# Kernel optimization log

Hardware: AMD Instinct MI355X
Metric: run time of the kernel (lower is better)

The kernel has to match this reference:

```python
import jax, jax.numpy as jnp
import numpy as np

N_CELLS = 50000
DEG = 32
NNZ = N_CELLS * DEG
D_IN = 64
D_OUT = 64
NEG_SLOPE = 0.2


def setup_inputs() -> dict:
    key = jax.random.key(0)
    k0, k1, k2, k3, k4 = jax.random.split(key, 5)
    x_source = jax.random.normal(k0, (N_CELLS, D_IN), jnp.float32)
    # COO indices of the sparse neighborhood matrix N: DEG entries per row
    edge_rows = jnp.repeat(jnp.arange(N_CELLS, dtype=jnp.int32), DEG)
    edge_cols = jax.random.randint(k1, (NNZ,), 0, N_CELLS, dtype=jnp.int32)
    neighborhood_values = jax.random.uniform(k2, (NNZ,), jnp.float32)
    # xavier_uniform-ish scales (exact init irrelevant for correctness baseline)
    W0 = jax.random.normal(k3, (D_IN, D_OUT), jnp.float32) * (1.414 / np.sqrt(D_IN))
    a0 = jax.random.normal(k4, (2 * D_OUT, 1), jnp.float32) * 0.1
    return {
        "x_source": x_source,
        "edge_rows": edge_rows,
        "edge_cols": edge_cols,
        "neighborhood_values": neighborhood_values,
        "W0": W0,
        "a0": a0,
    }


def reference(x_source, edge_rows, edge_cols, neighborhood_values, W0, a0):
    # message = X W_p  : [n_cells, d_out]
    message = x_source @ W0
    d = message.shape[1]
    # [X_i || X_j] a  ==  (X_i a_src) + (X_j a_dst); compute node-level dot first,
    # then gather per edge (avoids materializing [nnz, 2d] concat)
    a_src = a0[:d, 0]
    a_dst = a0[d:, 0]
    node_src = message @ a_src  # [n_cells]
    node_dst = message @ a_dst  # [n_cells]
    e = jax.nn.leaky_relu(node_src[edge_rows] + node_dst[edge_cols],
                          negative_slope=NEG_SLOPE)  # [nnz]
    # sparse_row_norm: divide each edge value by its row sum (softmax=False path)
    row_sum = jax.ops.segment_sum(e, edge_rows, num_segments=N_CELLS)
    att = e / row_sum[edge_rows]
    # Hadamard product N^1 \odot A_1, then SpMM with message
    vals = neighborhood_values * att  # [nnz]
    out = jax.ops.segment_sum(vals[:, None] * message[edge_cols], edge_rows,
                              num_segments=N_CELLS)  # [n_cells, d_out]
    # update_func='relu'
    return jax.nn.relu(out)
```

## Files before the change

kernel.cpp:

```cpp
#include <hip/hip_runtime.h>
#include <hip/hip_fp16.h>

#define N_CELLS 50000
#define DEG 32
#define DIM 64
#define NEG_SLOPE 0.2
#define NPAIRS (N_CELLS / 2)

__global__ __launch_bounds__(256)
void gat_prep(const float* __restrict__ x,
              const float* __restrict__ W0,
              const float* __restrict__ a0,
              __half* __restrict__ x2,
              double* __restrict__ ns,
              double* __restrict__ nd) {
  __shared__ double2 p_s[DIM];

  const int tid = threadIdx.x;
  if (tid < DIM) {
    double ps = 0.0, pd = 0.0;
    const float4* w4 = (const float4*)(W0 + tid * DIM);
#pragma unroll
    for (int q = 0; q < DIM / 4; ++q) {
      float4 w = w4[q];
      ps = fma((double)w.x, (double)a0[4 * q + 0], ps);
      ps = fma((double)w.y, (double)a0[4 * q + 1], ps);
      ps = fma((double)w.z, (double)a0[4 * q + 2], ps);
      ps = fma((double)w.w, (double)a0[4 * q + 3], ps);
      pd = fma((double)w.x, (double)a0[DIM + 4 * q + 0], pd);
      pd = fma((double)w.y, (double)a0[DIM + 4 * q + 1], pd);
      pd = fma((double)w.z, (double)a0[DIM + 4 * q + 2], pd);
      pd = fma((double)w.w, (double)a0[DIM + 4 * q + 3], pd);
    }
    p_s[tid] = make_double2(ps, pd);
  }
  __syncthreads();

  const int r = blockIdx.x * 256 + tid;
  if (r >= N_CELLS) return;

  const float4* x4 = (const float4*)(x + (size_t)r * DIM);
  double s0 = 0.0, s1 = 0.0, d0 = 0.0, d1 = 0.0;
  __half2 hbuf[DIM / 2];
#pragma unroll
  for (int q = 0; q < DIM / 4; ++q) {
    float4 v = x4[q];
    double2 p0 = p_s[4 * q + 0], p1 = p_s[4 * q + 1];
    double2 p2 = p_s[4 * q + 2], p3 = p_s[4 * q + 3];
    s0 = fma((double)v.x, p0.x, s0); d0 = fma((double)v.x, p0.y, d0);
    s1 = fma((double)v.y, p1.x, s1); d1 = fma((double)v.y, p1.y, d1);
    s0 = fma((double)v.z, p2.x, s0); d0 = fma((double)v.z, p2.y, d0);
    s1 = fma((double)v.w, p3.x, s1); d1 = fma((double)v.w, p3.y, d1);
    hbuf[2 * q + 0] = __float22half2_rn(make_float2(v.x, v.y));
    hbuf[2 * q + 1] = __float22half2_rn(make_float2(v.z, v.w));
  }
  ns[r] = s0 + s1;
  nd[r] = d0 + d1;

  const uint4* src = (const uint4*)hbuf;
  uint4* p2v = (uint4*)(x2 + (size_t)r * DIM);
#pragma unroll
  for (int i = 0; i < 8; ++i) p2v[i] = src[i];
}

__global__ __launch_bounds__(256, 4)
void gat_edges(const __half* __restrict__ x2,
               const int* __restrict__ ecol,
               const float* __restrict__ nv,
               const float* __restrict__ W0,
               const double* __restrict__ ns,
               const double* __restrict__ nd,
               float* __restrict__ out) {
  __shared__ __align__(16) float w_s[4][2][DEG];
  __shared__ __align__(16) int c_s[4][2][DEG];
  __shared__ __align__(16) float h_s[4][2][2][DIM];

  const int lane = threadIdx.x & 63;
  const int wid = threadIdx.x >> 6;
  const int half = lane >> 5;
  const int sub = lane & 31;

  float w0c[DIM];
#pragma unroll
  for (int k = 0; k < DIM; ++k) w0c[k] = W0[k * DIM + lane];

  const int gwave = blockIdx.x * 4 + wid;
  const int nwaves = gridDim.x * 4;
  const unsigned* xp = (const unsigned*)x2;

  int col_c = 0; float nv_c = 0.0f; double nd_c = 0.0, ns_c = 0.0;
  if (gwave < NPAIRS) {
    const int eidx = 2 * gwave * DEG + lane;
    col_c = __builtin_nontemporal_load(ecol + eidx);
    nv_c = __builtin_nontemporal_load(nv + eidx);
    nd_c = nd[col_c];
    ns_c = ns[2 * gwave + half];
  }

  int buf = 0;
  for (int p = gwave; p < NPAIRS; p += nwaves, buf ^= 1) {
    const int r0 = 2 * p;
    const int col = col_c;
    const float nvv = nv_c;
    const double ndv = nd_c;
    const double nsv = ns_c;

    double z = nsv + ndv;
    double e = (z >= 0.0) ? z : NEG_SLOPE * z;
    double rs = e;
#pragma unroll
    for (int m = 16; m >= 1; m >>= 1) rs += __shfl_xor(rs, m, 64);
    w_s[wid][half][sub] = nvv * ((float)e / (float)rs);
    c_s[wid][half][sub] = col;

    const int pn = p + nwaves;
    const int psafe = (pn < NPAIRS) ? pn : p;
    const int eidxn = 2 * psafe * DEG + lane;
    col_c = __builtin_nontemporal_load(ecol + eidxn);
    nv_c = __builtin_nontemporal_load(nv + eidxn);
    ns_c = ns[2 * psafe + half];

    const int* cs = c_s[wid][half];
    const float* wsp = w_s[wid][half];
    float ax = 0.0f, ay = 0.0f;
#pragma unroll
    for (int b = 0; b < DEG; b += 16) {
      unsigned pk[16];
#pragma unroll
      for (int i = 0; i < 16; ++i)
        pk[i] = xp[(size_t)cs[b + i] * (DIM / 2) + sub];
#pragma unroll
      for (int i = 0; i < 16; ++i) {
        float2 v = __half22float2(*(const __half2*)&pk[i]);
        float w = wsp[b + i];
        ax = fmaf(w, v.x, ax);
        ay = fmaf(w, v.y, ay);
      }
    }
    ((float2*)h_s[wid][buf][half])[sub] = make_float2(ax, ay);

    nd_c = nd[col_c];

    float oA = 0.0f, oB = 0.0f;
    const float4* hA = (const float4*)h_s[wid][buf][0];
    const float4* hB = (const float4*)h_s[wid][buf][1];
#pragma unroll
    for (int q = 0; q < DIM / 4; ++q) {
      float4 a = hA[q];
      float4 b = hB[q];
      oA = fmaf(a.x, w0c[4 * q + 0], oA); oB = fmaf(b.x, w0c[4 * q + 0], oB);
      oA = fmaf(a.y, w0c[4 * q + 1], oA); oB = fmaf(b.y, w0c[4 * q + 1], oB);
      oA = fmaf(a.z, w0c[4 * q + 2], oA); oB = fmaf(b.z, w0c[4 * q + 2], oB);
      oA = fmaf(a.w, w0c[4 * q + 3], oA); oB = fmaf(b.w, w0c[4 * q + 3], oB);
    }
    __builtin_nontemporal_store(fmaxf(oA, 0.0f), out + (size_t)r0 * DIM + lane);
    __builtin_nontemporal_store(fmaxf(oB, 0.0f), out + (size_t)(r0 + 1) * DIM + lane);
  }
}

extern "C" void kernel_launch(void* const* d_in, const int* in_sizes, int n_in,
                              void* d_out, int out_size, void* d_ws, size_t ws_size,
                              hipStream_t stream) {
  const float* x = (const float*)d_in[0];
  const int* ecol = (const int*)d_in[2];
  const float* nv = (const float*)d_in[3];
  const float* W0 = (const float*)d_in[4];
  const float* a0 = (const float*)d_in[5];
  float* out = (float*)d_out;

  __half* x2 = (__half*)d_ws;
  double* ns = (double*)((char*)d_ws + (size_t)N_CELLS * DIM * sizeof(__half));
  double* nd = ns + N_CELLS;

  hipLaunchKernelGGL(gat_prep, dim3((N_CELLS + 255) / 256), dim3(256), 0, stream,
                     x, W0, a0, x2, ns, nd);
  hipLaunchKernelGGL(gat_edges, dim3(1280), dim3(256), 0, stream,
                     x2, ecol, nv, W0, ns, nd, out);
}
```

Baseline: 120.6 us.

## Replace LDS staging in edge kernel with wave-uniform scalar loads and readlane broadcasts

Drops the shared-memory staging of edge weights, column indices and the aggregated hidden vector. Column indices now come as wave-uniform loads, weights and the aggregate are broadcast with readlane, and each lane gathers one half feature per neighbor instead of a packed half2. The goal is to remove LDS traffic and the associated waits. The cost is many serial readlane instructions, redundant reloads of ecol, and two-byte per-lane gathers instead of four-byte ones.

```diff
diff --git a/kernel.cpp b/kernel.cpp
--- a/kernel.cpp
+++ b/kernel.cpp
@@ -71,22 +71,16 @@
                const double* __restrict__ ns,
                const double* __restrict__ nd,
                float* __restrict__ out) {
-  __shared__ __align__(16) float w_s[4][2][DEG];
-  __shared__ __align__(16) int c_s[4][2][DEG];
-  __shared__ __align__(16) float h_s[4][2][2][DIM];
-
   const int lane = threadIdx.x & 63;
-  const int wid = threadIdx.x >> 6;
   const int half = lane >> 5;
-  const int sub = lane & 31;
 
   float w0c[DIM];
 #pragma unroll
   for (int k = 0; k < DIM; ++k) w0c[k] = W0[k * DIM + lane];
 
-  const int gwave = blockIdx.x * 4 + wid;
+  const int gwave =
+      __builtin_amdgcn_readfirstlane(blockIdx.x * 4 + (threadIdx.x >> 6));
   const int nwaves = gridDim.x * 4;
-  const unsigned* xp = (const unsigned*)x2;
 
   int col_c = 0; float nv_c = 0.0f; double nd_c = 0.0, ns_c = 0.0;
   if (gwave < NPAIRS) {
@@ -97,10 +91,8 @@
     ns_c = ns[2 * gwave + half];
   }
 
-  int buf = 0;
-  for (int p = gwave; p < NPAIRS; p += nwaves, buf ^= 1) {
+  for (int p = gwave; p < NPAIRS; p += nwaves) {
     const int r0 = 2 * p;
-    const int col = col_c;
     const float nvv = nv_c;
     const double ndv = nd_c;
     const double nsv = ns_c;
@@ -110,8 +102,7 @@
     double rs = e;
 #pragma unroll
     for (int m = 16; m >= 1; m >>= 1) rs += __shfl_xor(rs, m, 64);
-    w_s[wid][half][sub] = nvv * ((float)e / (float)rs);
-    c_s[wid][half][sub] = col;
+    const float wv = nvv * ((float)e / (float)rs);
 
     const int pn = p + nwaves;
     const int psafe = (pn < NPAIRS) ? pn : p;
@@ -120,41 +111,54 @@
     nv_c = __builtin_nontemporal_load(nv + eidxn);
     ns_c = ns[2 * psafe + half];
 
-    const int* cs = c_s[wid][half];
-    const float* wsp = w_s[wid][half];
-    float ax = 0.0f, ay = 0.0f;
 #pragma unroll
-    for (int b = 0; b < DEG; b += 16) {
-      unsigned pk[16];
+    for (int rr = 0; rr < 2; ++rr) {
+      const int r = r0 + rr;
+      float acc = 0.0f;
 #pragma unroll
-      for (int i = 0; i < 16; ++i)
-        pk[i] = xp[(size_t)cs[b + i] * (DIM / 2) + sub];
+      for (int b = 0; b < DEG; b += 16) {
+        int cj[16];
+        float wj[16];
+        float xf[16];
 #pragma unroll
-      for (int i = 0; i < 16; ++i) {
-        float2 v = __half22float2(*(const __half2*)&pk[i]);
-        float w = wsp[b + i];
-        ax = fmaf(w, v.x, ax);
-        ay = fmaf(w, v.y, ay);
+        for (int i = 0; i < 16; ++i)
+          cj[i] = ecol[r * DEG + b + i];
+#pragma unroll
+        for (int i = 0; i < 16; ++i)
+          wj[i] = __int_as_float(
+              __builtin_amdgcn_readlane(__float_as_int(wv), rr * 32 + b + i));
+#pragma unroll
+        for (int i = 0; i < 16; ++i)
+          xf[i] = __half2float(x2[(size_t)cj[i] * DIM + lane]);
+        float a0f = 0.0f, a1f = 0.0f, a2f = 0.0f, a3f = 0.0f;
+#pragma unroll
+        for (int i = 0; i < 16; i += 4) {
+          a0f = fmaf(wj[i + 0], xf[i + 0], a0f);
+          a1f = fmaf(wj[i + 1], xf[i + 1], a1f);
+          a2f = fmaf(wj[i + 2], xf[i + 2], a2f);
+          a3f = fmaf(wj[i + 3], xf[i + 3], a3f);
+        }
+        acc += (a0f + a1f) + (a2f + a3f);
       }
+
+      if (rr == 0) nd_c = nd[col_c];
+
+      float o0 = 0.0f, o1 = 0.0f, o2 = 0.0f, o3 = 0.0f;
+      const int acci = __float_as_int(acc);
+#pragma unroll
+      for (int k = 0; k < DIM; k += 4) {
+        o0 = fmaf(__int_as_float(__builtin_amdgcn_readlane(acci, k + 0)),
+                  w0c[k + 0], o0);
+        o1 = fmaf(__int_as_float(__builtin_amdgcn_readlane(acci, k + 1)),
+                  w0c[k + 1], o1);
+        o2 = fmaf(__int_as_float(__builtin_amdgcn_readlane(acci, k + 2)),
+                  w0c[k + 2], o2);
+        o3 = fmaf(__int_as_float(__builtin_amdgcn_readlane(acci, k + 3)),
+                  w0c[k + 3], o3);
+      }
+      const float o = (o0 + o1) + (o2 + o3);
+      __builtin_nontemporal_store(fmaxf(o, 0.0f), out + (size_t)r * DIM + lane);
     }
-    ((float2*)h_s[wid][buf][half])[sub] = make_float2(ax, ay);
-
-    nd_c = nd[col_c];
-
-    float oA = 0.0f, oB = 0.0f;
-    const float4* hA = (const float4*)h_s[wid][buf][0];
-    const float4* hB = (const float4*)h_s[wid][buf][1];
-#pragma unroll
-    for (int q = 0; q < DIM / 4; ++q) {
-      float4 a = hA[q];
-      float4 b = hB[q];
-      oA = fmaf(a.x, w0c[4 * q + 0], oA); oB = fmaf(b.x, w0c[4 * q + 0], oB);
-      oA = fmaf(a.y, w0c[4 * q + 1], oA); oB = fmaf(b.y, w0c[4 * q + 1], oB);
-      oA = fmaf(a.z, w0c[4 * q + 2], oA); oB = fmaf(b.z, w0c[4 * q + 2], oB);
-      oA = fmaf(a.w, w0c[4 * q + 3], oA); oB = fmaf(b.w, w0c[4 * q + 3], oB);
-    }
-    __builtin_nontemporal_store(fmaxf(oA, 0.0f), out + (size_t)r0 * DIM + lane);
-    __builtin_nontemporal_store(fmaxf(oB, 0.0f), out + (size_t)(r0 + 1) * DIM + lane);
   }
 }
 
```

After: 149.5 us. 1.24x slower.

## Precompute message X·W0 in separate kernel instead of applying W0 per edge-aggregate

Applied to the files above, without the earlier changes.

The W0 multiply moves out of the edge kernel. A new gat_msg kernel computes message = X·W0 once per node using readlane broadcasts and stores it as fp16. The edge kernel then aggregates the precomputed messages and writes them directly, with no LDS staging and no per-row 64x64 matvec. Column indices and weights are also read from LDS as vector loads. The cost is an extra kernel launch and an extra write and read of an fp16 node-sized array, and the fp16 rounding now applies to the message rather than to x.

```diff
diff --git a/kernel.cpp b/kernel.cpp
--- a/kernel.cpp
+++ b/kernel.cpp
@@ -8,12 +8,11 @@
 #define NPAIRS (N_CELLS / 2)
 
 __global__ __launch_bounds__(256)
-void gat_prep(const float* __restrict__ x,
-              const float* __restrict__ W0,
-              const float* __restrict__ a0,
-              __half* __restrict__ x2,
-              double* __restrict__ ns,
-              double* __restrict__ nd) {
+void gat_nodes(const float* __restrict__ x,
+               const float* __restrict__ W0,
+               const float* __restrict__ a0,
+               double* __restrict__ ns,
+               double* __restrict__ nd) {
   __shared__ double2 p_s[DIM];
 
   const int tid = threadIdx.x;
@@ -41,7 +40,6 @@
 
   const float4* x4 = (const float4*)(x + (size_t)r * DIM);
   double s0 = 0.0, s1 = 0.0, d0 = 0.0, d1 = 0.0;
-  __half2 hbuf[DIM / 2];
 #pragma unroll
   for (int q = 0; q < DIM / 4; ++q) {
     float4 v = x4[q];
@@ -51,42 +49,58 @@
     s1 = fma((double)v.y, p1.x, s1); d1 = fma((double)v.y, p1.y, d1);
     s0 = fma((double)v.z, p2.x, s0); d0 = fma((double)v.z, p2.y, d0);
     s1 = fma((double)v.w, p3.x, s1); d1 = fma((double)v.w, p3.y, d1);
-    hbuf[2 * q + 0] = __float22half2_rn(make_float2(v.x, v.y));
-    hbuf[2 * q + 1] = __float22half2_rn(make_float2(v.z, v.w));
   }
   ns[r] = s0 + s1;
   nd[r] = d0 + d1;
-
-  const uint4* src = (const uint4*)hbuf;
-  uint4* p2v = (uint4*)(x2 + (size_t)r * DIM);
-#pragma unroll
-  for (int i = 0; i < 8; ++i) p2v[i] = src[i];
 }
 
 __global__ __launch_bounds__(256, 4)
-void gat_edges(const __half* __restrict__ x2,
+void gat_msg(const float* __restrict__ x,
+             const float* __restrict__ W0,
+             __half* __restrict__ m2) {
+  const int lane = threadIdx.x & 63;
+
+  float w0c[DIM];
+#pragma unroll
+  for (int k = 0; k < DIM; ++k) w0c[k] = W0[k * DIM + lane];
+
+  const int gwave = blockIdx.x * 4 + (threadIdx.x >> 6);
+  const int nwaves = gridDim.x * 4;
+
+  for (int r = gwave; r < N_CELLS; r += nwaves) {
+    const float xv = x[(size_t)r * DIM + lane];
+    const int xi = __float_as_int(xv);
+    float m0 = 0.f, m1 = 0.f, m2a = 0.f, m3 = 0.f;
+#pragma unroll
+    for (int k = 0; k < DIM; k += 4) {
+      m0 = fmaf(__int_as_float(__builtin_amdgcn_readlane(xi, k + 0)), w0c[k + 0], m0);
+      m1 = fmaf(__int_as_float(__builtin_amdgcn_readlane(xi, k + 1)), w0c[k + 1], m1);
+      m2a = fmaf(__int_as_float(__builtin_amdgcn_readlane(xi, k + 2)), w0c[k + 2], m2a);
+      m3 = fmaf(__int_as_float(__builtin_amdgcn_readlane(xi, k + 3)), w0c[k + 3], m3);
+    }
+    const float m = (m0 + m1) + (m2a + m3);
+    m2[(size_t)r * DIM + lane] = __float2half(m);
+  }
+}
+
+__global__ __launch_bounds__(256, 4)
+void gat_edges(const __half* __restrict__ m2,
                const int* __restrict__ ecol,
                const float* __restrict__ nv,
-               const float* __restrict__ W0,
                const double* __restrict__ ns,
                const double* __restrict__ nd,
                float* __restrict__ out) {
   __shared__ __align__(16) float w_s[4][2][DEG];
   __shared__ __align__(16) int c_s[4][2][DEG];
-  __shared__ __align__(16) float h_s[4][2][2][DIM];
 
   const int lane = threadIdx.x & 63;
   const int wid = threadIdx.x >> 6;
   const int half = lane >> 5;
   const int sub = lane & 31;
 
-  float w0c[DIM];
-#pragma unroll
-  for (int k = 0; k < DIM; ++k) w0c[k] = W0[k * DIM + lane];
-
   const int gwave = blockIdx.x * 4 + wid;
   const int nwaves = gridDim.x * 4;
-  const unsigned* xp = (const unsigned*)x2;
+  const unsigned* xp = (const unsigned*)m2;
 
   int col_c = 0; float nv_c = 0.0f; double nd_c = 0.0, ns_c = 0.0;
   if (gwave < NPAIRS) {
@@ -97,10 +111,8 @@
     ns_c = ns[2 * gwave + half];
   }
 
-  int buf = 0;
-  for (int p = gwave; p < NPAIRS; p += nwaves, buf ^= 1) {
+  for (int p = gwave; p < NPAIRS; p += nwaves) {
     const int r0 = 2 * p;
-    const int col = col_c;
     const float nvv = nv_c;
     const double ndv = nd_c;
     const double nsv = ns_c;
@@ -111,7 +123,7 @@
 #pragma unroll
     for (int m = 16; m >= 1; m >>= 1) rs += __shfl_xor(rs, m, 64);
     w_s[wid][half][sub] = nvv * ((float)e / (float)rs);
-    c_s[wid][half][sub] = col;
+    c_s[wid][half][sub] = col_c;
 
     const int pn = p + nwaves;
     const int psafe = (pn < NPAIRS) ? pn : p;
@@ -125,36 +137,52 @@
     float ax = 0.0f, ay = 0.0f;
 #pragma unroll
     for (int b = 0; b < DEG; b += 16) {
+      const int4 ca = ((const int4*)(cs + b))[0];
+      const int4 cb = ((const int4*)(cs + b))[1];
+      const int4 cc = ((const int4*)(cs + b))[2];
+      const int4 cd = ((const int4*)(cs + b))[3];
+      const float4 wa = ((const float4*)(wsp + b))[0];
+      const float4 wb = ((const float4*)(wsp + b))[1];
+      const float4 wc = ((const float4*)(wsp + b))[2];
+      const float4 wd = ((const float4*)(wsp + b))[3];
       unsigned pk[16];
-#pragma unroll
-      for (int i = 0; i < 16; ++i)
-        pk[i] = xp[(size_t)cs[b + i] * (DIM / 2) + sub];
-#pragma unroll
-      for (int i = 0; i < 16; ++i) {
-        float2 v = __half22float2(*(const __half2*)&pk[i]);
-        float w = wsp[b + i];
-        ax = fmaf(w, v.x, ax);
-        ay = fmaf(w, v.y, ay);
+      pk[0]  = xp[(size_t)ca.x * (DIM / 2) + sub];
+      pk[1]  = xp[(size_t)ca.y * (DIM / 2) + sub];
+      pk[2]  = xp[(size_t)ca.z * (DIM / 2) + sub];
+      pk[3]  = xp[(size_t)ca.w * (DIM / 2) + sub];
+      pk[4]  = xp[(size_t)cb.x * (DIM / 2) + sub];
+      pk[5]  = xp[(size_t)cb.y * (DIM / 2) + sub];
+      pk[6]  = xp[(size_t)cb.z * (DIM / 2) + sub];
+      pk[7]  = xp[(size_t)cb.w * (DIM / 2) + sub];
+      pk[8]  = xp[(size_t)cc.x * (DIM / 2) + sub];
+      pk[9]  = xp[(size_t)cc.y * (DIM / 2) + sub];
+      pk[10] = xp[(size_t)cc.z * (DIM / 2) + sub];
+      pk[11] = xp[(size_t)cc.w * (DIM / 2) + sub];
+      pk[12] = xp[(size_t)cd.x * (DIM / 2) + sub];
+      pk[13] = xp[(size_t)cd.y * (DIM / 2) + sub];
+      pk[14] = xp[(size_t)cd.z * (DIM / 2) + sub];
+      pk[15] = xp[(size_t)cd.w * (DIM / 2) + sub];
+      float ax0 = 0.f, ay0 = 0.f, ax1 = 0.f, ay1 = 0.f;
+      const float wj[16] = {wa.x, wa.y, wa.z, wa.w, wb.x, wb.y, wb.z, wb.w,
+                            wc.x, wc.y, wc.z, wc.w, wd.x, wd.y, wd.z, wd.w};
+#pragma unroll
+      for (int i = 0; i < 16; i += 2) {
+        float2 v0 = __half22float2(*(const __half2*)&pk[i]);
+        float2 v1 = __half22float2(*(const __half2*)&pk[i + 1]);
+        ax0 = fmaf(wj[i], v0.x, ax0);
+        ay0 = fmaf(wj[i], v0.y, ay0);
+        ax1 = fmaf(wj[i + 1], v1.x, ax1);
+        ay1 = fmaf(wj[i + 1], v1.y, ay1);
       }
+      ax += ax0 + ax1;
+      ay += ay0 + ay1;
     }
-    ((float2*)h_s[wid][buf][half])[sub] = make_float2(ax, ay);
 
     nd_c = nd[col_c];
 
-    float oA = 0.0f, oB = 0.0f;
-    const float4* hA = (const float4*)h_s[wid][buf][0];
-    const float4* hB = (const float4*)h_s[wid][buf][1];
-#pragma unroll
-    for (int q = 0; q < DIM / 4; ++q) {
-      float4 a = hA[q];
-      float4 b = hB[q];
-      oA = fmaf(a.x, w0c[4 * q + 0], oA); oB = fmaf(b.x, w0c[4 * q + 0], oB);
-      oA = fmaf(a.y, w0c[4 * q + 1], oA); oB = fmaf(b.y, w0c[4 * q + 1], oB);
-      oA = fmaf(a.z, w0c[4 * q + 2], oA); oB = fmaf(b.z, w0c[4 * q + 2], oB);
-      oA = fmaf(a.w, w0c[4 * q + 3], oA); oB = fmaf(b.w, w0c[4 * q + 3], oB);
-    }
-    __builtin_nontemporal_store(fmaxf(oA, 0.0f), out + (size_t)r0 * DIM + lane);
-    __builtin_nontemporal_store(fmaxf(oB, 0.0f), out + (size_t)(r0 + 1) * DIM + lane);
+    const size_t o = (size_t)(r0 + half) * DIM + 2 * sub;
+    __builtin_nontemporal_store(fmaxf(ax, 0.0f), out + o);
+    __builtin_nontemporal_store(fmaxf(ay, 0.0f), out + o + 1);
   }
 }
 
@@ -168,12 +196,13 @@
   const float* a0 = (const float*)d_in[5];
   float* out = (float*)d_out;
 
-  __half* x2 = (__half*)d_ws;
+  __half* m2 = (__half*)d_ws;
   double* ns = (double*)((char*)d_ws + (size_t)N_CELLS * DIM * sizeof(__half));
   double* nd = ns + N_CELLS;
 
-  hipLaunchKernelGGL(gat_prep, dim3((N_CELLS + 255) / 256), dim3(256), 0, stream,
-                     x, W0, a0, x2, ns, nd);
+  hipLaunchKernelGGL(gat_nodes, dim3((N_CELLS + 255) / 256), dim3(256), 0, stream,
+                     x, W0, a0, ns, nd);
+  hipLaunchKernelGGL(gat_msg, dim3(800), dim3(256), 0, stream, x, W0, m2);
   hipLaunchKernelGGL(gat_edges, dim3(1280), dim3(256), 0, stream,
-                     x2, ecol, nv, W0, ns, nd, out);
-}
+                     m2, ecol, nv, ns, nd, out);
+}
```

Result: slower. 128.9 us (+6.9%).
